# Kernel tuning notes

Measured on AMD Instinct MI355X. Metric: run time of the kernel, lower is better.

The kernel has to match this reference:

```python
import jax, jax.numpy as jnp
import numpy as np

B, IDF, CDF, SIZE, H, L = 32, 64, 256, 32, 8, 256
SS = SIZE * SIZE  # size*size = 1024


def setup_inputs() -> dict:
    key = jax.random.key(0)
    k1, k2, k3 = jax.random.split(key, 3)
    return {
        "weightedContext": jax.random.normal(k1, (B, IDF, SS), dtype=jnp.float32),
        "context": jax.random.normal(k2, (B, CDF, L), dtype=jnp.float32),
        # per-head conv1x1 weights: [H, size*size, cdf]
        "W": jax.random.normal(k3, (H, SS, CDF), dtype=jnp.float32) * 0.02,
        "ih": SIZE,
        "iw": SIZE,
    }


def reference(weightedContext, context, W, ih, iw):
    batch, idf = weightedContext.shape[0], weightedContext.shape[1]
    # conv1x1 per head == per-head GEMM over channel dim: [B,H,SS,L]
    sourceC = jnp.einsum("hoc,bcl->bhol", W, context)
    # attention scores: [B,H,idf,L]
    attn = jnp.einsum("bio,bhol->bhil", weightedContext, sourceC)
    # softmax over sourceL (nn.Softmax() on 2D view -> dim=1 == L here)
    attn = jax.nn.softmax(attn, axis=-1)
    # weightedContext_T summed over heads: bmm(sourceC, attn^T) -> [B,idf,SS]
    ctx_out = jnp.einsum("bhol,bhil->bio", sourceC, attn)
    ctx_out = ctx_out.reshape(batch, idf, ih, iw)
    # attnOut: per-head attn transposed [B,L,idf], summed over heads
    attn_out = jnp.sum(attn, axis=1).transpose(0, 2, 1)
    return ctx_out, attn_out
```

## Files before the change

### kernel.cpp

```cpp
#include <hip/hip_runtime.h>
#include <hip/hip_bf16.h>

#define BB 32
#define IDF 64
#define CDF 256
#define SSZ 1024
#define NH 8
#define LL 256
#define KHC 2048

typedef __attribute__((ext_vector_type(8))) _Float16 half8v;
typedef __attribute__((ext_vector_type(4))) float f32x4;

#define GLDS16(g, l) __builtin_amdgcn_global_load_lds(                        \
    (const __attribute__((address_space(1))) void*)(g),                       \
    (__attribute__((address_space(3))) void*)(l), 16, 0, 0)

#define WAIT_ENTER3(NFULL, NHALF)                                             \
  { if (ks < NSTEP - 2)                                                       \
      asm volatile("s_waitcnt vmcnt(" #NFULL ")" ::: "memory");               \
    else if (ks == NSTEP - 2)                                                 \
      asm volatile("s_waitcnt vmcnt(" #NHALF ")" ::: "memory");               \
    else                                                                      \
      asm volatile("s_waitcnt vmcnt(0)" ::: "memory");                        \
    __builtin_amdgcn_s_barrier();                                             \
    __builtin_amdgcn_sched_barrier(0); }
#define WAIT_P1()                                                             \
  { if (ks < NSTEP - 2) {                                                     \
      if (wave < 4) asm volatile("s_waitcnt vmcnt(6)" ::: "memory");          \
      else          asm volatile("s_waitcnt vmcnt(4)" ::: "memory");          \
    } else if (ks == NSTEP - 2) {                                             \
      if (wave < 4) asm volatile("s_waitcnt vmcnt(3)" ::: "memory");          \
      else          asm volatile("s_waitcnt vmcnt(2)" ::: "memory");          \
    } else asm volatile("s_waitcnt vmcnt(0)" ::: "memory");                   \
    __builtin_amdgcn_s_barrier();                                             \
    __builtin_amdgcn_sched_barrier(0); }
#define BAR_EXIT()                                                            \
  { __builtin_amdgcn_sched_barrier(0);                                        \
    __builtin_amdgcn_s_barrier();                                             \
    __builtin_amdgcn_sched_barrier(0); }
#define LDS_BAR()                                                             \
  { asm volatile("s_waitcnt lgkmcnt(0)" ::: "memory");                        \
    __builtin_amdgcn_s_barrier();                                             \
    __builtin_amdgcn_sched_barrier(0); }

__device__ inline unsigned short f2h(float x) {
  _Float16 h = (_Float16)x;
  return *reinterpret_cast<unsigned short*>(&h);
}
__device__ inline float h2f(unsigned short u) {
  _Float16 h = *reinterpret_cast<_Float16*>(&u);
  return (float)h;
}

__global__ __launch_bounds__(256) void k_prep(const float* __restrict__ wc,
                                              const float* __restrict__ W,
                                              const float* __restrict__ ctx,
                                              unsigned short* __restrict__ wc16,
                                              unsigned short* __restrict__ W16,
                                              unsigned short* __restrict__ ctx16,
                                              unsigned short* __restrict__ Wt16,
                                              unsigned short* __restrict__ cT16) {
  __shared__ float Tt[64][65];
  int blk0 = blockIdx.x;
  int t = threadIdx.x;
  if (blk0 < 6144) {
    int sel = blk0 >> 11;
    int idx = ((blk0 & 2047) * 256 + t) * 4;
    const float* src = (sel == 0) ? wc : (sel == 1) ? W : ctx;
    unsigned short* d = (sel == 0) ? wc16 : (sel == 1) ? W16 : ctx16;
    float4 v = *reinterpret_cast<const float4*>(&src[idx]);
    __align__(8) unsigned short h[4] = {f2h(v.x), f2h(v.y), f2h(v.z), f2h(v.w)};
    *reinterpret_cast<int2*>(&d[idx]) = *reinterpret_cast<int2*>(h);
  } else if (blk0 < 6656) {
    int blk = blk0 - 6144;
    int h = blk >> 6, ot = (blk >> 2) & 15, cq = blk & 3;
    int og = ot * 64, cg = cq * 64;
    int o_l = t >> 4, c4 = (t & 15) * 4;
#pragma unroll
    for (int p = 0; p < 4; ++p) {
      int o = o_l + 16 * p;
      float4 v = *reinterpret_cast<const float4*>(
          &W[((size_t)h * SSZ + og + o) * CDF + cg + c4]);
      Tt[c4 + 0][o] = v.x; Tt[c4 + 1][o] = v.y;
      Tt[c4 + 2][o] = v.z; Tt[c4 + 3][o] = v.w;
    }
    __syncthreads();
    int c_l = t >> 2;
#pragma unroll
    for (int p = 0; p < 4; ++p) {
      int o0 = ((t & 3) + 4 * p) * 4;
      __align__(8) unsigned short hv[4];
#pragma unroll
      for (int j = 0; j < 4; ++j) hv[j] = f2h(Tt[c_l][o0 + j]);
      size_t base = ((size_t)h * CDF + cg + c_l) * SSZ + og + o0;
      *reinterpret_cast<int2*>(&Wt16[base]) = *reinterpret_cast<int2*>(hv);
    }
  } else {
    int blk = blk0 - 6656;
    int b = blk >> 4, cq = (blk >> 2) & 3, lt = blk & 3;
    int cg = cq * 64, lg = lt * 64;
    int c_l = t >> 4, l4 = (t & 15) * 4;
#pragma unroll
    for (int p = 0; p < 4; ++p) {
      int c = c_l + 16 * p;
      float4 v = *reinterpret_cast<const float4*>(
          &ctx[((size_t)b * CDF + cg + c) * LL + lg + l4]);
      Tt[l4 + 0][c] = v.x; Tt[l4 + 1][c] = v.y;
      Tt[l4 + 2][c] = v.z; Tt[l4 + 3][c] = v.w;
    }
    __syncthreads();
    int l_l = t >> 2;
#pragma unroll
    for (int p = 0; p < 4; ++p) {
      int c0 = ((t & 3) + 4 * p) * 4;
      __align__(8) unsigned short hv[4];
#pragma unroll
      for (int j = 0; j < 4; ++j) hv[j] = f2h(Tt[l_l][c0 + j]);
      size_t base = ((size_t)b * LL + lg + l_l) * CDF + cg + c0;
      *reinterpret_cast<int2*>(&cT16[base]) = *reinterpret_cast<int2*>(hv);
    }
  }
}

#define BUFS 10240

__device__ __forceinline__ void st_p1(short* dst, const short* gA, const short* gB,
                                      int wave, int lane, int k0) {
  if (wave < 4) {
    int r = wave * 16 + (lane >> 2);
    int gc = (lane & 3) ^ ((r >> 1) & 3);
    GLDS16(gA + (size_t)r * SSZ + k0 + gc * 8, dst + wave * 512);
  }
#pragma unroll
  for (int j = 0; j < 2; ++j) {
    int bi = wave * 2 + j;
    int brow = bi * 16 + (lane >> 2);
    int gc = (lane & 3) ^ ((brow >> 1) & 3);
    GLDS16(gB + (size_t)brow * SSZ + k0 + gc * 8, dst + 2048 + bi * 512);
  }
}
__device__ __forceinline__ void st_p23(short* dst, const short* gB, int ld,
                                       int wave, int lane, int k0) {
#pragma unroll
  for (int j = 0; j < 2; ++j) {
    int inst = wave * 2 + j;
    int brow = inst * 16 + (lane >> 2);
    int gc = (lane & 3) ^ ((brow >> 1) & 3);
    GLDS16(gB + (size_t)brow * ld + k0 + gc * 8, dst + inst * 512);
  }
}

__global__ __launch_bounds__(512) void k123(const unsigned short* __restrict__ wc16,
                                            const unsigned short* __restrict__ Wt16,
                                            const unsigned short* __restrict__ cT16,
                                            const unsigned short* __restrict__ ctx16,
                                            unsigned short* __restrict__ P16,
                                            unsigned short* __restrict__ N216) {
  __shared__ __align__(16) short S[3 * BUFS + 16384];
  short* P_lds = &S[3 * BUFS];

  int blk = blockIdx.x;
  int b = blk >> 3, h = blk & 7;
  int t = threadIdx.x;
  int lane = t & 63, wave = t >> 6;
  int g = wave >> 2, w4 = wave & 3;
  int ln15 = lane & 15, kh = lane >> 4;
  int rowq = (lane >> 4) * 4;

  const short* gA = (const short*)wc16 + (size_t)b * IDF * SSZ;
  const short* gB = (const short*)Wt16 + (size_t)h * CDF * SSZ;
  const short* gT = (const short*)cT16 + (size_t)b * LL * CDF;
  const short* gC = (const short*)ctx16 + (size_t)b * CDF * LL;

  int offA[2], rowM[2], rmask[2];
#pragma unroll
  for (int r = 0; r < 2; ++r) {
    int row = g * 32 + r * 16 + ln15;
    offA[r] = row * 32 + ((kh ^ ((row >> 1) & 3)) * 8);
    rowM[r] = row * 256;
    rmask[r] = row & 7;
  }
  int offB1[4], offB2[4];
#pragma unroll
  for (int c = 0; c < 4; ++c) {
    int row = w4 * 64 + c * 16 + ln15;
    int swz = ((kh ^ ((row >> 1) & 3)) * 8);
    offB1[c] = 2048 + row * 32 + swz;
    offB2[c] = row * 32 + swz;
  }

  f32x4 acc[2][4] = {};

  st_p1(&S[0],        gA, gB, wave, lane, 0);
  st_p1(&S[BUFS],     gA, gB, wave, lane, 32);
  st_p1(&S[2 * BUFS], gA, gB, wave, lane, 64);
  int cur = 0;
  {
    const int NSTEP = 32;
#pragma unroll 1
    for (int ks = 0; ks < NSTEP; ++ks) {
      short* Sc = &S[cur * BUFS];
      WAIT_P1()
      half8v fa[2], fb[4];
#pragma unroll
      for (int r = 0; r < 2; ++r)
        fa[r] = *reinterpret_cast<const half8v*>(&Sc[offA[r]]);
#pragma unroll
      for (int c = 0; c < 4; ++c)
        fb[c] = *reinterpret_cast<const half8v*>(&Sc[offB1[c]]);
      __builtin_amdgcn_s_setprio(1);
#pragma unroll
      for (int r = 0; r < 2; ++r)
#pragma unroll
        for (int c = 0; c < 4; ++c)
          acc[r][c] = __builtin_amdgcn_mfma_f32_16x16x32_f16(fa[r], fb[c], acc[r][c], 0, 0, 0);
      __builtin_amdgcn_s_setprio(0);
      BAR_EXIT()
      if (ks + 3 < NSTEP)
        st_p1(Sc, gA, gB, wave, lane, (ks + 3) * 32);
      cur = (cur == 2) ? 0 : cur + 1;
    }
  }
#pragma unroll
  for (int r = 0; r < 2; ++r)
#pragma unroll
    for (int c = 0; c < 4; ++c)
#pragma unroll
      for (int reg = 0; reg < 4; ++reg) {
        int row = g * 32 + r * 16 + rowq + reg;
        int col = w4 * 64 + c * 16 + ln15;
        P_lds[row * 256 + ((((col >> 3) ^ (row & 7)) << 3) + (col & 7))] =
            (short)f2h(acc[r][c][reg]);
      }
  LDS_BAR()

#pragma unroll
  for (int r = 0; r < 2; ++r)
#pragma unroll
    for (int c = 0; c < 4; ++c) acc[r][c] = (f32x4){0.f, 0.f, 0.f, 0.f};
  st_p23(&S[0],        gT, CDF, wave, lane, 0);
  st_p23(&S[BUFS],     gT, CDF, wave, lane, 32);
  st_p23(&S[2 * BUFS], gT, CDF, wave, lane, 64);
  cur = 0;
  {
    const int NSTEP = 8;
#pragma unroll 1
    for (int ks = 0; ks < NSTEP; ++ks) {
      short* Sc = &S[cur * BUFS];
      WAIT_ENTER3(4, 2)
      half8v fa[2], fb[4];
#pragma unroll
      for (int r = 0; r < 2; ++r) {
        int ck = ((ks * 4 + kh) ^ rmask[r]) << 3;
        fa[r] = *reinterpret_cast<const half8v*>(&P_lds[rowM[r] + ck]);
      }
#pragma unroll
      for (int c = 0; c < 4; ++c)
        fb[c] = *reinterpret_cast<const half8v*>(&Sc[offB2[c]]);
      __builtin_amdgcn_s_setprio(1);
#pragma unroll
      for (int r = 0; r < 2; ++r)
#pragma unroll
        for (int c = 0; c < 4; ++c)
          acc[r][c] = __builtin_amdgcn_mfma_f32_16x16x32_f16(fa[r], fb[c], acc[r][c], 0, 0, 0);
      __builtin_amdgcn_s_setprio(0);
      BAR_EXIT()
      if (ks + 3 < NSTEP)
        st_p23(Sc, gT, CDF, wave, lane, (ks + 3) * 32);
      cur = (cur == 2) ? 0 : cur + 1;
    }
  }

  st_p23(&S[0],        gC, LL, wave, lane, 0);
  st_p23(&S[BUFS],     gC, LL, wave, lane, 32);
  st_p23(&S[2 * BUFS], gC, LL, wave, lane, 64);

  float* pm = reinterpret_cast<float*>(P_lds);
  float gmax[2][4], ginv[2][4];
#pragma unroll
  for (int r = 0; r < 2; ++r)
#pragma unroll
    for (int reg = 0; reg < 4; ++reg) {
      float m = fmaxf(fmaxf(acc[r][0][reg], acc[r][1][reg]),
                      fmaxf(acc[r][2][reg], acc[r][3][reg]));
#pragma unroll
      for (int msk = 8; msk >= 1; msk >>= 1) m = fmaxf(m, __shfl_xor(m, msk, 64));
      if (ln15 == 0) pm[(g * 32 + r * 16 + rowq + reg) * 4 + w4] = m;
    }
  LDS_BAR()
#pragma unroll
  for (int r = 0; r < 2; ++r)
#pragma unroll
    for (int reg = 0; reg < 4; ++reg) {
      int row = g * 32 + r * 16 + rowq + reg;
      float4 p0 = *reinterpret_cast<const float4*>(&pm[row * 4]);
      gmax[r][reg] = fmaxf(fmaxf(p0.x, p0.y), fmaxf(p0.z, p0.w));
    }
  LDS_BAR()
#pragma unroll
  for (int r = 0; r < 2; ++r)
#pragma unroll
    for (int reg = 0; reg < 4; ++reg) {
      float s = 0.f;
#pragma unroll
      for (int c = 0; c < 4; ++c) {
        acc[r][c][reg] = __expf(acc[r][c][reg] - gmax[r][reg]);
        s += acc[r][c][reg];
      }
#pragma unroll
      for (int msk = 8; msk >= 1; msk >>= 1) s += __shfl_xor(s, msk, 64);
      if (ln15 == 0) pm[(g * 32 + r * 16 + rowq + reg) * 4 + w4] = s;
    }
  LDS_BAR()
#pragma unroll
  for (int r = 0; r < 2; ++r)
#pragma unroll
    for (int reg = 0; reg < 4; ++reg) {
      int row = g * 32 + r * 16 + rowq + reg;
      float4 p0 = *reinterpret_cast<const float4*>(&pm[row * 4]);
      ginv[r][reg] = 1.f / (p0.x + p0.y + p0.z + p0.w);
    }
  LDS_BAR()

  size_t pbase = (size_t)blk * IDF * LL;
#pragma unroll
  for (int r = 0; r < 2; ++r)
#pragma unroll
    for (int c = 0; c < 4; ++c)
#pragma unroll
      for (int reg = 0; reg < 4; ++reg) {
        float p = acc[r][c][reg] * ginv[r][reg];
        int row = g * 32 + r * 16 + rowq + reg;
        int col = w4 * 64 + c * 16 + ln15;
        unsigned short ph = f2h(p);
        P16[pbase + (size_t)row * LL + col] = ph;
        P_lds[row * 256 + ((((col >> 3) ^ (row & 7)) << 3) + (col & 7))] = (short)ph;
      }
  LDS_BAR()

#pragma unroll
  for (int r = 0; r < 2; ++r)
#pragma unroll
    for (int c = 0; c < 4; ++c) acc[r][c] = (f32x4){0.f, 0.f, 0.f, 0.f};
  cur = 0;
  {
    const int NSTEP = 8;
#pragma unroll 1
    for (int ks = 0; ks < NSTEP; ++ks) {
      short* Sc = &S[cur * BUFS];
      WAIT_ENTER3(4, 2)
      half8v fa[2], fb[4];
#pragma unroll
      for (int r = 0; r < 2; ++r) {
        int ck = ((ks * 4 + kh) ^ rmask[r]) << 3;
        fa[r] = *reinterpret_cast<const half8v*>(&P_lds[rowM[r] + ck]);
      }
#pragma unroll
      for (int c = 0; c < 4; ++c)
        fb[c] = *reinterpret_cast<const half8v*>(&Sc[offB2[c]]);
      __builtin_amdgcn_s_setprio(1);
#pragma unroll
      for (int r = 0; r < 2; ++r)
#pragma unroll
        for (int c = 0; c < 4; ++c)
          acc[r][c] = __builtin_amdgcn_mfma_f32_16x16x32_f16(fa[r], fb[c], acc[r][c], 0, 0, 0);
      __builtin_amdgcn_s_setprio(0);
      BAR_EXIT()
      if (ks + 3 < NSTEP)
        st_p23(Sc, gC, LL, wave, lane, (ks + 3) * 32);
      cur = (cur == 2) ? 0 : cur + 1;
    }
  }

  size_t nbase = (size_t)b * IDF * KHC + h * CDF;
#pragma unroll
  for (int r = 0; r < 2; ++r)
#pragma unroll
    for (int c = 0; c < 4; ++c)
#pragma unroll
      for (int reg = 0; reg < 4; ++reg) {
        int row = g * 32 + r * 16 + rowq + reg;
        int col = w4 * 64 + c * 16 + ln15;
        N216[nbase + (size_t)row * KHC + col] = f2h(acc[r][c][reg]);
      }
}

__device__ __forceinline__ void k4_stage(short* dst,
                                         const short* gA0, const short* gA1,
                                         const short* gW,
                                         int wave, int lane, int kk0, int obase) {
  int h4 = kk0 >> 8, cb = kk0 & 255;
#pragma unroll
  for (int j = 0; j < 2; ++j) {
    int inst = wave * 2 + j;
    if (inst < 8) {
      int gi = inst >> 2;
      int rb = (inst & 3) * 16;
      int r  = rb + (lane >> 2);
      int gc = (lane & 3) ^ ((r >> 1) & 3);
      const short* src = gi ? gA1 : gA0;
      GLDS16(src + (size_t)r * KHC + kk0 + gc * 8, dst + gi * 2048 + rb * 32);
    } else {
      int bi = inst - 8;
      int brow = bi * 16 + (lane >> 2);
      int gc = (lane & 3) ^ ((brow >> 1) & 3);
      GLDS16(gW + (size_t)(h4 * SSZ + obase + brow) * CDF + cb + gc * 8,
             dst + 4096 + bi * 512);
    }
  }
}

__global__ __launch_bounds__(512) void k4_mfma(const unsigned short* __restrict__ N216,
                                               const unsigned short* __restrict__ W16,
                                               const unsigned short* __restrict__ P16,
                                               float* __restrict__ out0,
                                               float* __restrict__ out1,
                                               float* __restrict__ outa) {
  __shared__ __align__(16) short S[3 * 8192];

  int blk = blockIdx.x;
  int t = threadIdx.x;

  if (blk >= 256) {
    int bblk = blk - 256;
    int b = bblk >> 2, lt = bblk & 3;
    int l0 = lt * 64;
    float* T = reinterpret_cast<float*>(S);
    float4 acc2[2];
#pragma unroll
    for (int p = 0; p < 2; ++p) acc2[p] = make_float4(0.f, 0.f, 0.f, 0.f);
    for (int h = 0; h < NH; ++h) {
      size_t src = (size_t)(b * NH + h) * IDF * LL;
#pragma unroll
      for (int p = 0; p < 2; ++p) {
        int f = t + p * 512;
        int i = f >> 4, lc = (f & 15) * 4;
        ushort4 u = *reinterpret_cast<const ushort4*>(&P16[src + i * LL + l0 + lc]);
        acc2[p].x += h2f(u.x); acc2[p].y += h2f(u.y);
        acc2[p].z += h2f(u.z); acc2[p].w += h2f(u.w);
      }
    }
#pragma unroll
    for (int p = 0; p < 2; ++p) {
      int f = t + p * 512;
      int i = f >> 4, lc = (f & 15) * 4;
      T[i * 65 + lc + 0] = acc2[p].x; T[i * 65 + lc + 1] = acc2[p].y;
      T[i * 65 + lc + 2] = acc2[p].z; T[i * 65 + lc + 3] = acc2[p].w;
    }
    __syncthreads();
#pragma unroll
    for (int p = 0; p < 2; ++p) {
      int f = t + p * 512;
      int lr = f >> 4, ic = (f & 15) * 4;
      float4 v = {T[(ic + 0) * 65 + lr], T[(ic + 1) * 65 + lr],
                  T[(ic + 2) * 65 + lr], T[(ic + 3) * 65 + lr]};
      *reinterpret_cast<float4*>(&outa[((size_t)b * LL + l0 + lr) * IDF + ic]) = v;
    }
    return;
  }

  int g = blk >> 7;
  int r7 = blk & 127;
  int bp = r7 >> 3, ot = r7 & 7;
  int obase = ot * 128;
  int lane = t & 63, wave = t >> 6;
  int gr = wave >> 2, w4 = wave & 3;
  int ln15 = lane & 15, kh = lane >> 4;

  int b = bp * 2 + gr;
  const short* gA0 = (const short*)N216 + (size_t)(bp * 2 + 0) * IDF * KHC;
  const short* gA1 = (const short*)N216 + (size_t)(bp * 2 + 1) * IDF * KHC;
  const short* gW  = (const short*)W16;

  int offA[4], offB[2];
#pragma unroll
  for (int r = 0; r < 4; ++r) {
    int row = r * 16 + ln15;
    offA[r] = gr * 2048 + row * 32 + ((kh ^ ((row >> 1) & 3)) * 8);
  }
#pragma unroll
  for (int c = 0; c < 2; ++c) {
    int row = w4 * 32 + c * 16 + ln15;
    offB[c] = 4096 + row * 32 + ((kh ^ ((row >> 1) & 3)) * 8);
  }

  int kbase = g * (KHC / 2);
  f32x4 acc[4][2] = {};

  k4_stage(&S[0],        gA0, gA1, gW, wave, lane, kbase, obase);
  k4_stage(&S[8192],     gA0, gA1, gW, wave, lane, kbase + 32, obase);
  k4_stage(&S[2 * 8192], gA0, gA1, gW, wave, lane, kbase + 64, obase);
  int cur = 0;

  const int NSTEP = 32;
#pragma unroll 1
  for (int ks = 0; ks < NSTEP; ++ks) {
    short* Sc = &S[cur * 8192];
    WAIT_ENTER3(4, 2)
    half8v fa[4], fb[2];
#pragma unroll
    for (int r = 0; r < 4; ++r)
      fa[r] = *reinterpret_cast<const half8v*>(&Sc[offA[r]]);
#pragma unroll
    for (int c = 0; c < 2; ++c)
      fb[c] = *reinterpret_cast<const half8v*>(&Sc[offB[c]]);
    __builtin_amdgcn_s_setprio(1);
#pragma unroll
    for (int r = 0; r < 4; ++r)
#pragma unroll
      for (int c = 0; c < 2; ++c)
        acc[r][c] = __builtin_amdgcn_mfma_f32_16x16x32_f16(fa[r], fb[c], acc[r][c], 0, 0, 0);
    __builtin_amdgcn_s_setprio(0);
    BAR_EXIT()
    if (ks + 3 < NSTEP)
      k4_stage(Sc, gA0, gA1, gW, wave, lane, kbase + (ks + 3) * 32, obase);
    cur = (cur == 2) ? 0 : cur + 1;
  }

  float* dst = (g == 0) ? out0 : out1;
  int rowq = (lane >> 4) * 4;
#pragma unroll
  for (int r = 0; r < 4; ++r)
#pragma unroll
    for (int c = 0; c < 2; ++c)
#pragma unroll
      for (int reg = 0; reg < 4; ++reg)
        dst[((size_t)b * IDF + r * 16 + rowq + reg) * SSZ +
            obase + w4 * 32 + c * 16 + ln15] = acc[r][c][reg];
}

__global__ __launch_bounds__(256) void k_add(float* __restrict__ out,
                                             const float* __restrict__ Pbuf) {
  int idx = blockIdx.x * 256 + threadIdx.x;
  float4 a = reinterpret_cast<float4*>(out)[idx];
  float4 p = reinterpret_cast<const float4*>(Pbuf)[idx];
  a.x += p.x; a.y += p.y; a.z += p.z; a.w += p.w;
  reinterpret_cast<float4*>(out)[idx] = a;
}

extern "C" void kernel_launch(void* const* d_in, const int* in_sizes, int n_in,
                              void* d_out, int out_size, void* d_ws, size_t ws_size,
                              hipStream_t stream) {
  const float* wc  = (const float*)d_in[0];
  const float* ctx = (const float*)d_in[1];
  const float* W   = (const float*)d_in[2];
  float* out = (float*)d_out;

  const size_t NE = 2097152;
  const size_t NM = 4194304;
  unsigned short* p = (unsigned short*)d_ws;
  unsigned short *wc16 = p;   p += NE;
  unsigned short *Wt16 = p;   p += NE;
  unsigned short *W16  = p;   p += NE;
  unsigned short *ctx16 = p;  p += NE;
  unsigned short *cT16 = p;   p += NE;
  unsigned short *P16  = p;   p += NM;
  unsigned short *N216 = p;   p += NM;
  float* Pbuf = (float*)p;

  k_prep  <<<7168, 256, 0, stream>>>(wc, W, ctx, wc16, W16, ctx16, Wt16, cT16);
  k123    <<<256, 512, 0, stream>>>(wc16, Wt16, cT16, ctx16, P16, N216);
  k4_mfma <<<384, 512, 0, stream>>>(N216, W16, P16, out, Pbuf,
                                    out + (size_t)BB * IDF * SSZ);
  k_add   <<<2048, 256, 0, stream>>>(out, Pbuf);
}
```

Before: 75.09 us.

## Fuse fp16 casts into transpose blocks and replace split-K add with atomics

The prep kernel now writes the plain fp16 copies of W and context from the same loads it uses for the transposes, dropping the separate cast blocks that reread those tensors. It also zero-fills the main output in prep. The final GEMM then accumulates both split-K halves into that output with float atomicAdd, which removes the partial buffer and the extra k_add launch. This saves a kernel launch and a full read/write pass over the output, at the cost of atomic traffic and a summation order that is no longer deterministic.

```diff
diff --git a/kernel.cpp b/kernel.cpp
--- a/kernel.cpp
+++ b/kernel.cpp
@@ -60,28 +60,28 @@
                                               unsigned short* __restrict__ W16,
                                               unsigned short* __restrict__ ctx16,
                                               unsigned short* __restrict__ Wt16,
-                                              unsigned short* __restrict__ cT16) {
+                                              unsigned short* __restrict__ cT16,
+                                              float* __restrict__ outz) {
   __shared__ float Tt[64][65];
   int blk0 = blockIdx.x;
   int t = threadIdx.x;
-  if (blk0 < 6144) {
-    int sel = blk0 >> 11;
-    int idx = ((blk0 & 2047) * 256 + t) * 4;
-    const float* src = (sel == 0) ? wc : (sel == 1) ? W : ctx;
-    unsigned short* d = (sel == 0) ? wc16 : (sel == 1) ? W16 : ctx16;
-    float4 v = *reinterpret_cast<const float4*>(&src[idx]);
+  if (blk0 < 2048) {
+    int idx = (blk0 * 256 + t) * 4;
+    float4 v = *reinterpret_cast<const float4*>(&wc[idx]);
     __align__(8) unsigned short h[4] = {f2h(v.x), f2h(v.y), f2h(v.z), f2h(v.w)};
-    *reinterpret_cast<int2*>(&d[idx]) = *reinterpret_cast<int2*>(h);
-  } else if (blk0 < 6656) {
-    int blk = blk0 - 6144;
+    *reinterpret_cast<int2*>(&wc16[idx]) = *reinterpret_cast<int2*>(h);
+  } else if (blk0 < 2560) {
+    int blk = blk0 - 2048;
     int h = blk >> 6, ot = (blk >> 2) & 15, cq = blk & 3;
     int og = ot * 64, cg = cq * 64;
     int o_l = t >> 4, c4 = (t & 15) * 4;
 #pragma unroll
     for (int p = 0; p < 4; ++p) {
       int o = o_l + 16 * p;
-      float4 v = *reinterpret_cast<const float4*>(
-          &W[((size_t)h * SSZ + og + o) * CDF + cg + c4]);
+      size_t gidx = ((size_t)h * SSZ + og + o) * CDF + cg + c4;
+      float4 v = *reinterpret_cast<const float4*>(&W[gidx]);
+      __align__(8) unsigned short hv[4] = {f2h(v.x), f2h(v.y), f2h(v.z), f2h(v.w)};
+      *reinterpret_cast<int2*>(&W16[gidx]) = *reinterpret_cast<int2*>(hv);
       Tt[c4 + 0][o] = v.x; Tt[c4 + 1][o] = v.y;
       Tt[c4 + 2][o] = v.z; Tt[c4 + 3][o] = v.w;
     }
@@ -96,16 +96,18 @@
       size_t base = ((size_t)h * CDF + cg + c_l) * SSZ + og + o0;
       *reinterpret_cast<int2*>(&Wt16[base]) = *reinterpret_cast<int2*>(hv);
     }
-  } else {
-    int blk = blk0 - 6656;
+  } else if (blk0 < 3072) {
+    int blk = blk0 - 2560;
     int b = blk >> 4, cq = (blk >> 2) & 3, lt = blk & 3;
     int cg = cq * 64, lg = lt * 64;
     int c_l = t >> 4, l4 = (t & 15) * 4;
 #pragma unroll
     for (int p = 0; p < 4; ++p) {
       int c = c_l + 16 * p;
-      float4 v = *reinterpret_cast<const float4*>(
-          &ctx[((size_t)b * CDF + cg + c) * LL + lg + l4]);
+      size_t gidx = ((size_t)b * CDF + cg + c) * LL + lg + l4;
+      float4 v = *reinterpret_cast<const float4*>(&ctx[gidx]);
+      __align__(8) unsigned short hv[4] = {f2h(v.x), f2h(v.y), f2h(v.z), f2h(v.w)};
+      *reinterpret_cast<int2*>(&ctx16[gidx]) = *reinterpret_cast<int2*>(hv);
       Tt[l4 + 0][c] = v.x; Tt[l4 + 1][c] = v.y;
       Tt[l4 + 2][c] = v.z; Tt[l4 + 3][c] = v.w;
     }
@@ -120,6 +122,9 @@
       size_t base = ((size_t)b * LL + lg + l_l) * CDF + cg + c0;
       *reinterpret_cast<int2*>(&cT16[base]) = *reinterpret_cast<int2*>(hv);
     }
+  } else {
+    int idx = ((blk0 - 3072) * 256 + t) * 4;
+    *reinterpret_cast<float4*>(&outz[idx]) = make_float4(0.f, 0.f, 0.f, 0.f);
   }
 }
 
@@ -415,7 +420,6 @@
                                                const unsigned short* __restrict__ W16,
                                                const unsigned short* __restrict__ P16,
                                                float* __restrict__ out0,
-                                               float* __restrict__ out1,
                                                float* __restrict__ outa) {
   __shared__ __align__(16) short S[3 * 8192];
 
@@ -518,7 +522,6 @@
     cur = (cur == 2) ? 0 : cur + 1;
   }
 
-  float* dst = (g == 0) ? out0 : out1;
   int rowq = (lane >> 4) * 4;
 #pragma unroll
   for (int r = 0; r < 4; ++r)
@@ -526,17 +529,8 @@
     for (int c = 0; c < 2; ++c)
 #pragma unroll
       for (int reg = 0; reg < 4; ++reg)
-        dst[((size_t)b * IDF + r * 16 + rowq + reg) * SSZ +
-            obase + w4 * 32 + c * 16 + ln15] = acc[r][c][reg];
-}
-
-__global__ __launch_bounds__(256) void k_add(float* __restrict__ out,
-                                             const float* __restrict__ Pbuf) {
-  int idx = blockIdx.x * 256 + threadIdx.x;
-  float4 a = reinterpret_cast<float4*>(out)[idx];
-  float4 p = reinterpret_cast<const float4*>(Pbuf)[idx];
-  a.x += p.x; a.y += p.y; a.z += p.z; a.w += p.w;
-  reinterpret_cast<float4*>(out)[idx] = a;
+        atomicAdd(&out0[((size_t)b * IDF + r * 16 + rowq + reg) * SSZ +
+                        obase + w4 * 32 + c * 16 + ln15], acc[r][c][reg]);
 }
 
 extern "C" void kernel_launch(void* const* d_in, const int* in_sizes, int n_in,
@@ -557,11 +551,9 @@
   unsigned short *cT16 = p;   p += NE;
   unsigned short *P16  = p;   p += NM;
   unsigned short *N216 = p;   p += NM;
-  float* Pbuf = (float*)p;
-
-  k_prep  <<<7168, 256, 0, stream>>>(wc, W, ctx, wc16, W16, ctx16, Wt16, cT16);
+
+  k_prep  <<<5120, 256, 0, stream>>>(wc, W, ctx, wc16, W16, ctx16, Wt16, cT16, out);
   k123    <<<256, 512, 0, stream>>>(wc16, Wt16, cT16, ctx16, P16, N216);
-  k4_mfma <<<384, 512, 0, stream>>>(N216, W16, P16, out, Pbuf,
+  k4_mfma <<<384, 512, 0, stream>>>(N216, W16, P16, out,
                                     out + (size_t)BB * IDF * SSZ);
-  k_add   <<<2048, 256, 0, stream>>>(out, Pbuf);
-}
+}
```

After: 77.36 us. 3.0% more time.
